# Kernel optimization log

Hardware: AMD Instinct MI355X
Metric: run time of the kernel (lower is better)

## Reference

```python
import jax, jax.numpy as jnp
import numpy as np

NUM_HEADS = 8
LN_EPS = 1e-5


def _avg_pool_mat(n_in, n_out):
    # torch adaptive_avg_pool windows: start=floor(i*n_in/n_out), end=ceil((i+1)*n_in/n_out)
    M = np.zeros((n_out, n_in), dtype=np.float32)
    for i in range(n_out):
        s = (i * n_in) // n_out
        e = -((-(i + 1) * n_in) // n_out)
        M[i, s:e] = 1.0 / (e - s)
    return jnp.asarray(M)


def _adaptive_avg_pool(x, out_hw):
    # separable mean over rectangular windows: [B,C,H,W] -> [B,C,out,out]
    Mh = _avg_pool_mat(x.shape[2], out_hw)
    Mw = _avg_pool_mat(x.shape[3], out_hw)
    return jnp.einsum('bchw,ph,qw->bcpq', x, Mh, Mw)


def _max_pool(x, oh, ow):
    # exact (divisible) adaptive max pool
    B, C, H, W = x.shape
    assert H % oh == 0 and W % ow == 0
    return x.reshape(B, C, oh, H // oh, ow, W // ow).max(axis=(3, 5))


def _conv1x1_res(t, w, b):
    # t + Conv2d(1x1)(t); w is [C_in, C_out]
    return t + jnp.einsum('bchw,cd->bdhw', t, w) + b[None, :, None, None]


def _tokens(t):
    B, C = t.shape[:2]
    return t.reshape(B, C, -1).transpose(0, 2, 1)  # [B, hw, C]


def setup_inputs():
    B, L, C = 8, 1024, 512
    H = W = 64
    key = jax.random.key(0)
    ks = jax.random.split(key, 16)
    n = lambda k, s, sc=0.02: jax.random.normal(k, s, jnp.float32) * sc
    return dict(
        x=jax.random.normal(ks[0], (B, H * W, C), jnp.float32),
        m=jax.random.normal(ks[1], (B, L, C), jnp.float32),
        w_s1=n(ks[2], (C, C)), b_s1=n(ks[3], (C,)),
        w_s2=n(ks[4], (C, C)), b_s2=n(ks[5], (C,)),
        w_s3=n(ks[6], (C, C)), b_s3=n(ks[7], (C,)),
        w_s4=n(ks[8], (C, C)), b_s4=n(ks[9], (C,)),
        w_mx=n(ks[10], (C, C)), b_mx=n(ks[11], (C,)),
        ln_g=jnp.ones((C,), jnp.float32), ln_b=jnp.zeros((C,), jnp.float32),
        Wq=n(ks[12], (C, C)), Wkv=n(ks[13], (C, 2 * C)),
        Wp=n(ks[14], (C, C)), bp=n(ks[15], (C,)),
        H=H, W=W, patch_size=16,
    )


def reference(x, m, w_s1, b_s1, w_s2, b_s2, w_s3, b_s3, w_s4, b_s4,
              w_mx, b_mx, ln_g, ln_b, Wq, Wkv, Wp, bp, H, W, patch_size):
    B, L, C = m.shape
    nh = NUM_HEADS
    d = C // nh
    scale = d ** -0.5

    q = (m @ Wq).reshape(B, L, nh, d).transpose(0, 2, 1, 3)  # [B,nh,L,d]

    x_ = x.transpose(0, 2, 1).reshape(B, C, H, W)
    s1 = _conv1x1_res(_adaptive_avg_pool(x_, round(H * 4 / 12)), w_s1, b_s1)
    s2 = _conv1x1_res(_adaptive_avg_pool(x_, round(H * 4 / 16)), w_s2, b_s2)
    s3 = _conv1x1_res(_adaptive_avg_pool(x_, round(H * 4 / 20)), w_s3, b_s3)
    s4 = _conv1x1_res(_adaptive_avg_pool(x_, round(H * 4 / 24)), w_s4, b_s4)
    mx = _conv1x1_res(_max_pool(x_, H * 4 // patch_size, W * 4 // patch_size), w_mx, b_mx)

    p = jnp.concatenate([_tokens(s1), _tokens(s2), _tokens(s3), _tokens(s4), _tokens(mx)], axis=1)
    mu = p.mean(-1, keepdims=True)
    var = ((p - mu) ** 2).mean(-1, keepdims=True)
    p = (p - mu) / jnp.sqrt(var + LN_EPS) * ln_g + ln_b

    kv_in = jnp.concatenate([p, m], axis=1)  # [B, N_p+L, C]
    kv = (kv_in @ Wkv).reshape(B, -1, 2, nh, d)
    k = kv[:, :, 0].transpose(0, 2, 1, 3)  # [B,nh,N,d]
    v = kv[:, :, 1].transpose(0, 2, 1, 3)

    attn = jax.nn.softmax(jnp.einsum('bhld,bhnd->bhln', q, k) * scale, axis=-1)
    out = jnp.einsum('bhln,bhnd->bhld', attn, v).transpose(0, 2, 1, 3).reshape(B, L, C)
    out = out @ Wp + bp
    return out, mx
```

## Files before the change

### kernel.cpp

```cpp
#include <hip/hip_runtime.h>

typedef unsigned short u16;
typedef __attribute__((ext_vector_type(8))) short bf16x8;
typedef __attribute__((ext_vector_type(4))) float f32x4;

__device__ __forceinline__ float bf2f(u16 u) {
  union { unsigned int i; float f; } x; x.i = ((unsigned int)u) << 16; return x.f;
}
__device__ __forceinline__ u16 f2bf(float f) {
  union { float f; unsigned int i; } x; x.f = f;
  unsigned int r = x.i + 0x7fffu + ((x.i >> 16) & 1u);
  return (u16)(r >> 16);
}

#define CFENCE() asm volatile("" ::: "memory")

__global__ __launch_bounds__(256) void k_pool(
    const float* __restrict__ x, u16* __restrict__ pool)
{
  int blk = blockIdx.x;
  int b = blk / 1243;
  int tok = blk - b * 1243;
  int c = threadIdx.x;
  const float* xb = x + (size_t)b * 4096 * 512;
  float r0, r1;
  if (tok >= 987) {
    int t = tok - 987;
    int oh = t >> 4, ow = t & 15;
    float m0 = -1e38f, m1 = -1e38f;
    for (int hh = 0; hh < 4; hh++)
      for (int ww = 0; ww < 4; ww++) {
        const float* px = xb + (size_t)((oh * 4 + hh) * 64 + ow * 4 + ww) * 512 + c;
        m0 = fmaxf(m0, px[0]);
        m1 = fmaxf(m1, px[256]);
      }
    r0 = m0; r1 = m1;
  } else {
    int n, t;
    if (tok < 441)      { n = 21; t = tok; }
    else if (tok < 697) { n = 16; t = tok - 441; }
    else if (tok < 866) { n = 13; t = tok - 697; }
    else                { n = 11; t = tok - 866; }
    int oh = t / n, ow = t - oh * n;
    int h0 = (oh * 64) / n, h1 = ((oh + 1) * 64 + n - 1) / n;
    int w0 = (ow * 64) / n, w1 = ((ow + 1) * 64 + n - 1) / n;
    float inv = 1.0f / (float)((h1 - h0) * (w1 - w0));
    float s0 = 0.f, s1 = 0.f;
    for (int hh = h0; hh < h1; hh++)
      for (int ww = w0; ww < w1; ww++) {
        const float* px = xb + (size_t)(hh * 64 + ww) * 512 + c;
        s0 += px[0];
        s1 += px[256];
      }
    r0 = s0 * inv; r1 = s1 * inv;
  }
  u16* dst = pool + (size_t)(b * 1243 + tok) * 512 + c;
  dst[0]   = f2bf(r0);
  dst[256] = f2bf(r1);
}

__global__ __launch_bounds__(256) void k_wt8(
    const float* w0, const float* w1, const float* w2, const float* w3,
    const float* w4, const float* w5, const float* w6, const float* w7,
    u16* __restrict__ wt_base)
{
  int z = blockIdx.z;
  int N = (z == 6) ? 1024 : 512;
  if (N == 512 && blockIdx.x >= 16) return;
  const float* W =
      z == 0 ? w0 : z == 1 ? w1 : z == 2 ? w2 : z == 3 ? w3 :
      z == 4 ? w4 : z == 5 ? w5 : z == 6 ? w6 : w7;
  size_t doff = (z <= 5) ? (size_t)z * 262144
                         : (z == 6 ? (size_t)6 * 262144 : (size_t)6 * 262144 + 524288);
  u16* Wt = wt_base + doff;

  __shared__ float tile[32][33];
  int n0 = blockIdx.x * 32, k0 = blockIdx.y * 32;
  int t = threadIdx.x;
  int rr = t >> 5, cc = t & 31;
#pragma unroll
  for (int ps = 0; ps < 4; ps++)
    tile[ps * 8 + rr][cc] = W[(size_t)(k0 + ps * 8 + rr) * N + n0 + cc];
  __syncthreads();
#pragma unroll
  for (int ps = 0; ps < 4; ps++)
    Wt[(size_t)(n0 + ps * 8 + rr) * 512 + k0 + cc] = f2bf(tile[cc][ps * 8 + rr]);
}

__global__ __launch_bounds__(256) void k_f2b(
    const float* __restrict__ src, u16* __restrict__ dst)
{
  size_t i = ((size_t)blockIdx.x * 256 + threadIdx.x) * 8;
  float4 a = *(const float4*)(src + i);
  float4 b = *(const float4*)(src + i + 4);
  ushort4 u0, u1;
  u0.x = f2bf(a.x); u0.y = f2bf(a.y); u0.z = f2bf(a.z); u0.w = f2bf(a.w);
  u1.x = f2bf(b.x); u1.y = f2bf(b.y); u1.z = f2bf(b.z); u1.w = f2bf(b.w);
  *(ushort4*)(dst + i) = u0;
  *(ushort4*)(dst + i + 4) = u1;
}

template <class EPI>
__device__ __forceinline__ void gemm_core(
    const u16* __restrict__ Az, const u16* __restrict__ Bt,
    int M, int K, int m0, int n0, EPI&& epi)
{
  __shared__ __align__(16) u16 As[128][40];
  __shared__ __align__(16) u16 Bs[128][40];

  const int tid = threadIdx.x;
  const int lane = tid & 63, wv = tid >> 6;
  const int quad = lane >> 4, l15 = lane & 15;
  const int wm = (wv >> 1) * 64, wn = (wv & 1) * 64;

  f32x4 acc[4][4];
#pragma unroll
  for (int i = 0; i < 4; i++)
#pragma unroll
    for (int j = 0; j < 4; j++) acc[i][j] = (f32x4){0.f, 0.f, 0.f, 0.f};

  const int srow = tid >> 1;
  const int scol = (tid & 1) * 16;
  const bool aok = (m0 + srow) < M;
  const u16* ag = Az + (size_t)(m0 + srow) * K + scol;
  const u16* bg = Bt + (size_t)(n0 + srow) * K + scol;

  uint4 a0 = {0, 0, 0, 0}, a1 = {0, 0, 0, 0}, b0, b1;
  if (aok) { a0 = *(const uint4*)ag; a1 = *(const uint4*)(ag + 8); }
  b0 = *(const uint4*)bg;
  b1 = *(const uint4*)(bg + 8);

  for (int k0 = 0; k0 < K; k0 += 32) {
    CFENCE();
    __builtin_amdgcn_s_barrier();
    asm volatile("s_waitcnt vmcnt(0)" ::: "memory");
    *(uint4*)&As[srow][scol]     = a0;
    *(uint4*)&As[srow][scol + 8] = a1;
    *(uint4*)&Bs[srow][scol]     = b0;
    *(uint4*)&Bs[srow][scol + 8] = b1;
    if (k0 + 32 < K) {
      if (aok) { a0 = *(const uint4*)(ag + k0 + 32); a1 = *(const uint4*)(ag + k0 + 40); }
      b0 = *(const uint4*)(bg + k0 + 32);
      b1 = *(const uint4*)(bg + k0 + 40);
    }
    asm volatile("s_waitcnt lgkmcnt(0)" ::: "memory");
    __builtin_amdgcn_s_barrier();
    CFENCE();

    bf16x8 af[4];
#pragma unroll
    for (int i = 0; i < 4; i++)
      af[i] = *(const bf16x8*)&As[wm + i * 16 + l15][quad * 8];
#pragma unroll
    for (int j = 0; j < 4; j++) {
      bf16x8 bfj = *(const bf16x8*)&Bs[wn + j * 16 + l15][quad * 8];
#pragma unroll
      for (int i = 0; i < 4; i++)
        acc[i][j] = __builtin_amdgcn_mfma_f32_16x16x32_bf16(af[i], bfj, acc[i][j], 0, 0, 0);
    }
  }

#pragma unroll
  for (int i = 0; i < 4; i++) {
    int rb = m0 + wm + i * 16 + quad * 4;
#pragma unroll
    for (int j = 0; j < 4; j++) {
      int col = n0 + wn + j * 16 + l15;
#pragma unroll
      for (int r = 0; r < 4; r++) {
        int row = rb + r;
        if (row >= M) continue;
        epi(row, col, acc[i][j][r]);
      }
    }
  }
}

__global__ __launch_bounds__(256) void k_gemm_bf(
    const u16* __restrict__ A, long long a_bs, const u16* __restrict__ Bt,
    u16* __restrict__ C, long long c_bs, int M, int N, int K)
{
  const u16* Az = A + (size_t)blockIdx.z * a_bs;
  u16* Cz = C + (size_t)blockIdx.z * c_bs;
  gemm_core(Az, Bt, M, K, blockIdx.y * 128, blockIdx.x * 128,
            [&](int row, int col, float v) {
              Cz[(size_t)row * N + col] = f2bf(v);
            });
}

__global__ __launch_bounds__(256) void k_gemm_f32(
    const u16* __restrict__ A, long long a_bs, const u16* __restrict__ Bt,
    const float* __restrict__ bias, float* __restrict__ C, long long c_bs,
    int M, int N, int K)
{
  const u16* Az = A + (size_t)blockIdx.z * a_bs;
  float* Cz = C + (size_t)blockIdx.z * c_bs;
  gemm_core(Az, Bt, M, K, blockIdx.y * 128, blockIdx.x * 128,
            [&](int row, int col, float v) {
              Cz[(size_t)row * N + col] = v + bias[col];
            });
}

__global__ __launch_bounds__(256) void k_gemm_qkv(
    const u16* __restrict__ mb, const u16* __restrict__ Bt,
    u16* __restrict__ q, u16* __restrict__ KV)
{
  int bz = blockIdx.z;
  const u16* Az = mb + (size_t)bz * (1024 * 512);
  u16* qz  = q  + (size_t)bz * (1024 * 512);
  u16* kvz = KV + (size_t)(bz * 2267 + 1243) * 1024;
  gemm_core(Az, Bt, 1024, 512, blockIdx.y * 128, blockIdx.x * 128,
            [&](int row, int col, float v) {
              u16 bv = f2bf(v);
              if (col < 512) qz[(size_t)row * 512 + col] = bv;
              else           kvz[(size_t)row * 1024 + (col - 512)] = bv;
            });
}

__global__ __launch_bounds__(256) void k_conv_seg(
    const u16* __restrict__ pool, const u16* __restrict__ wts,
    const float* b0, const float* b1, const float* b2, const float* b3,
    const float* b4, u16* __restrict__ p)
{
  int y = blockIdx.y;
  int s, m0;
  if (y < 4)      { s = 0; m0 = y * 128; }
  else if (y < 6) { s = 1; m0 = (y - 4) * 128; }
  else if (y < 8) { s = 2; m0 = (y - 6) * 128; }
  else if (y < 9) { s = 3; m0 = 0; }
  else            { s = 4; m0 = (y - 9) * 128; }
  int t0  = s == 0 ? 0 : s == 1 ? 441 : s == 2 ? 697 : s == 3 ? 866 : 987;
  int cnt = s == 0 ? 441 : s == 1 ? 256 : s == 2 ? 169 : s == 3 ? 121 : 256;
  const float* bias = s == 0 ? b0 : s == 1 ? b1 : s == 2 ? b2 : s == 3 ? b3 : b4;
  size_t base = (size_t)blockIdx.z * (1243 * 512) + (size_t)t0 * 512;
  const u16* Az = pool + base;
  u16* Cz = p + base;
  gemm_core(Az, wts + (size_t)s * 262144, cnt, 512, m0, blockIdx.x * 128,
            [&](int row, int col, float v) {
              v += bias[col] + bf2f(Az[(size_t)row * 512 + col]);
              Cz[(size_t)row * 512 + col] = f2bf(v);
            });
}

__global__ __launch_bounds__(256) void k_ln(
    u16* __restrict__ p, const float* __restrict__ g, const float* __restrict__ bb)
{
  __shared__ float red[8];
  size_t row = blockIdx.x;
  u16* pr = p + row * 512;
  int t = threadIdx.x;
  float v0 = bf2f(pr[t]), v1 = bf2f(pr[t + 256]);
  float s = v0 + v1;
#pragma unroll
  for (int off = 1; off < 64; off <<= 1) s += __shfl_xor(s, off);
  int wave = t >> 6;
  if ((t & 63) == 0) red[wave] = s;
  __syncthreads();
  float mean = (red[0] + red[1] + red[2] + red[3]) * (1.f / 512.f);
  float d0 = v0 - mean, d1 = v1 - mean;
  float s2 = d0 * d0 + d1 * d1;
#pragma unroll
  for (int off = 1; off < 64; off <<= 1) s2 += __shfl_xor(s2, off);
  if ((t & 63) == 0) red[4 + wave] = s2;
  __syncthreads();
  float var = (red[4] + red[5] + red[6] + red[7]) * (1.f / 512.f);
  float rstd = rsqrtf(var + 1e-5f);
  pr[t]       = f2bf(d0 * rstd * g[t]       + bb[t]);
  pr[t + 256] = f2bf(d1 * rstd * g[t + 256] + bb[t + 256]);
}

__global__ __launch_bounds__(256) void k_mxout(
    const u16* __restrict__ p, float* __restrict__ out2)
{
  __shared__ float tile[64][65];
  int tt = blockIdx.x;
  int cc = blockIdx.y;
  int b  = blockIdx.z;
  int tid = threadIdx.x;
  for (int rep = 0; rep < 16; rep++) {
    int e = rep * 256 + tid;
    int r = e >> 6, c = e & 63;
    tile[r][c] = bf2f(p[((size_t)(b * 1243 + 987 + tt * 64 + r)) * 512 + cc * 64 + c]);
  }
  __syncthreads();
  for (int rep = 0; rep < 16; rep++) {
    int e = rep * 256 + tid;
    int crow = e >> 6, tpos = e & 63;
    out2[((size_t)(b * 512 + cc * 64 + crow)) * 256 + tt * 64 + tpos] = tile[tpos][crow];
  }
}

__global__ __launch_bounds__(512) void k_attn_mfma(
    const u16* __restrict__ qb, const u16* __restrict__ KV,
    u16* __restrict__ outb)
{
  __shared__ __align__(16) u16 smem[4][64][72];
#define Qs_ (smem[0])
#define Ks_ (smem[1])
#define Vt_ (smem[2])
#define Ps_ (smem[3])

  const int bid = blockIdx.x;
  const int qt = bid >> 6;
  const int hb = bid & 63;
  const int h = hb & 7, b = hb >> 3;
  const int tid = threadIdx.x;
  const int lane = tid & 63, wv = tid >> 6;
  const int qw = wv >> 1, kw = wv & 1;
  const int quad = lane >> 4, l15 = lane & 15;

  const u16* kvb = KV + (size_t)b * 2267 * 1024;
  const int kr = tid >> 3, kc = (tid & 7) * 8;
  const int vp = tid & 31, vc = (tid >> 5) * 4;

  uint4 kreg = {0, 0, 0, 0};
  uint2 vra = {0, 0}, vrb = {0, 0};
  auto load_tile = [&](int n0) {
    kreg = (uint4){0, 0, 0, 0};
    vra = (uint2){0, 0};
    vrb = (uint2){0, 0};
    if (n0 + kr < 2267)
      kreg = *(const uint4*)(kvb + (size_t)(n0 + kr) * 1024 + h * 64 + kc);
    int na = n0 + 2 * vp;
    const u16* s = kvb + (size_t)na * 1024 + 512 + h * 64 + vc;
    if (na < 2267)     vra = *(const uint2*)s;
    if (na + 1 < 2267) vrb = *(const uint2*)(s + 1024);
  };

  load_tile(0);
  {
    int r = tid >> 3, c = (tid & 7) * 8;
    *(uint4*)&Qs_[r][c] =
        *(const uint4*)(qb + (size_t)(b * 1024 + qt * 64 + r) * 512 + h * 64 + c);
  }

  float l_lane[4];
  f32x4 o_acc[4];
#pragma unroll
  for (int i = 0; i < 4; i++) { l_lane[i] = 0.f; o_acc[i] = (f32x4){0.f, 0.f, 0.f, 0.f}; }

  __syncthreads();

  for (int n0 = 0; n0 < 2267; n0 += 64) {
    CFENCE();
    __builtin_amdgcn_s_barrier();
    asm volatile("s_waitcnt vmcnt(0)" ::: "memory");
    *(uint4*)&Ks_[kr][kc] = kreg;
    {
      unsigned lo0 = __builtin_amdgcn_perm(vrb.x, vra.x, 0x05040100u);
      unsigned hi0 = __builtin_amdgcn_perm(vrb.x, vra.x, 0x07060302u);
      unsigned lo1 = __builtin_amdgcn_perm(vrb.y, vra.y, 0x05040100u);
      unsigned hi1 = __builtin_amdgcn_perm(vrb.y, vra.y, 0x07060302u);
      *(unsigned*)&Vt_[vc + 0][2 * vp] = lo0;
      *(unsigned*)&Vt_[vc + 1][2 * vp] = hi0;
      *(unsigned*)&Vt_[vc + 2][2 * vp] = lo1;
      *(unsigned*)&Vt_[vc + 3][2 * vp] = hi1;
    }
    if (n0 + 64 < 2267) load_tile(n0 + 64);
    asm volatile("s_waitcnt lgkmcnt(0)" ::: "memory");
    __builtin_amdgcn_s_barrier();
    CFENCE();

    bf16x8 aq0 = *(const bf16x8*)&Qs_[qw * 16 + l15][quad * 8];
    bf16x8 aq1 = *(const bf16x8*)&Qs_[qw * 16 + l15][32 + quad * 8];
    f32x4 sacc[2];
#pragma unroll
    for (int t = 0; t < 2; t++) {
      int krow = kw * 32 + t * 16 + l15;
      bf16x8 bk0 = *(const bf16x8*)&Ks_[krow][quad * 8];
      bf16x8 bk1 = *(const bf16x8*)&Ks_[krow][32 + quad * 8];
      f32x4 z = (f32x4){0.f, 0.f, 0.f, 0.f};
      z = __builtin_amdgcn_mfma_f32_16x16x32_bf16(aq0, bk0, z, 0, 0, 0);
      sacc[t] = __builtin_amdgcn_mfma_f32_16x16x32_bf16(aq1, bk1, z, 0, 0, 0);
    }

#pragma unroll
    for (int r = 0; r < 4; r++) {
      float ls = 0.f;
#pragma unroll
      for (int t = 0; t < 2; t++) {
        float e = __builtin_amdgcn_exp2f(fminf(sacc[t][r] * 0.18033688f, 43.28f));
        ls += e;
        Ps_[qw * 16 + quad * 4 + r][kw * 32 + t * 16 + l15] = f2bf(e);
      }
      l_lane[r] += ls;
    }

    bf16x8 ap = *(const bf16x8*)&Ps_[qw * 16 + l15][kw * 32 + quad * 8];
#pragma unroll
    for (int t = 0; t < 4; t++) {
      bf16x8 vf = *(const bf16x8*)&Vt_[t * 16 + l15][kw * 32 + quad * 8];
      o_acc[t] = __builtin_amdgcn_mfma_f32_16x16x32_bf16(ap, vf, o_acc[t], 0, 0, 0);
    }
  }

  float lw[4];
#pragma unroll
  for (int r = 0; r < 4; r++) {
    float l = l_lane[r];
#pragma unroll
    for (int off = 1; off < 16; off <<= 1) l += __shfl_xor(l, off);
    lw[r] = l;
  }

  __syncthreads();
  float* Op = (float*)&smem[0][0][0];
  float* Lp = (float*)&smem[2][0][0];
  if (kw == 1) {
#pragma unroll
    for (int t = 0; t < 4; t++)
#pragma unroll
      for (int r = 0; r < 4; r++)
        Op[(qw * 16 + quad * 4 + r) * 64 + t * 16 + l15] = o_acc[t][r];
    if (l15 == 0) {
#pragma unroll
      for (int r = 0; r < 4; r++) Lp[qw * 16 + quad * 4 + r] = lw[r];
    }
  }
  __syncthreads();
  if (kw == 0) {
#pragma unroll
    for (int r = 0; r < 4; r++) {
      int row = qw * 16 + quad * 4 + r;
      float l = lw[r] + Lp[row] - 37.f;
      float inv = 1.f / fmaxf(l, 1e-20f);
#pragma unroll
      for (int t = 0; t < 4; t++) {
        size_t oi = (size_t)(b * 1024 + qt * 64 + row) * 512 + h * 64 + t * 16 + l15;
        outb[oi] = f2bf((o_acc[t][r] + Op[row * 64 + t * 16 + l15]) * inv);
      }
    }
  }
#undef Qs_
#undef Ks_
#undef Vt_
#undef Ps_
}

extern "C" void kernel_launch(void* const* d_in, const int* in_sizes, int n_in,
                              void* d_out, int out_size, void* d_ws, size_t ws_size,
                              hipStream_t stream)
{
  const float* x = (const float*)d_in[0];
  const float* m = (const float*)d_in[1];
  const float* ln_g = (const float*)d_in[12];
  const float* ln_b = (const float*)d_in[13];
  const float* Wq   = (const float*)d_in[14];
  const float* Wkv  = (const float*)d_in[15];
  const float* Wp   = (const float*)d_in[16];
  const float* bp   = (const float*)d_in[17];
  float* out = (float*)d_out;

  u16* pool = (u16*)d_ws;
  u16* p    = pool + 5091328;
  u16* q    = p + 5091328;
  u16* KV   = q + 4194304;
  u16* mb   = KV + 18571264;
  u16* wt_s = mb + 4194304;
  u16* attn_out = pool;

  k_wt8<<<dim3(32, 16, 8), 256, 0, stream>>>(
      (const float*)d_in[2], (const float*)d_in[4], (const float*)d_in[6],
      (const float*)d_in[8], (const float*)d_in[10], Wq, Wkv, Wp, wt_s);
  k_f2b<<<2048, 256, 0, stream>>>(m, mb);

  k_pool<<<9944, 256, 0, stream>>>(x, pool);

  k_conv_seg<<<dim3(4, 11, 8), 256, 0, stream>>>(
      pool, wt_s, (const float*)d_in[3], (const float*)d_in[5],
      (const float*)d_in[7], (const float*)d_in[9], (const float*)d_in[11], p);

  k_mxout<<<dim3(4, 8, 8), 256, 0, stream>>>(p, out + 4194304);
  k_ln<<<9944, 256, 0, stream>>>(p, ln_g, ln_b);

  k_gemm_qkv<<<dim3(12, 8, 8), 256, 0, stream>>>(mb, wt_s + 5 * 262144, q, KV);

  k_gemm_bf<<<dim3(8, 10, 8), 256, 0, stream>>>(p, (long long)1243 * 512,
                                                wt_s + 6 * 262144,
                                                KV, (long long)2267 * 1024,
                                                1243, 1024, 512);

  k_attn_mfma<<<1024, 512, 0, stream>>>(q, KV, attn_out);

  k_gemm_f32<<<dim3(4, 8, 8), 256, 0, stream>>>(attn_out, (long long)1024 * 512,
                                                wt_s + 6 * 262144 + 524288, bp,
                                                out, (long long)1024 * 512,
                                                1024, 512, 512);
  (void)in_sizes; (void)n_in; (void)out_size; (void)ws_size;
}
```

Before: 412.4 us.

## Fuse small launches and streamline attention softmax with DPP transposes

Folds the m-to-bf16 conversion into the pooling launch, writes the transposed max-pool output straight from the conv epilogue, and merges the QKV and pooled-KV GEMMs into one launch, removing three kernel launches and a separate transpose pass. In attention, Q fragments are loaded directly into registers instead of through shared memory, and the probability tile is packed with DPP quad transposes plus v_cvt_pk_bf16 into wider LDS stores, with a cheaper row-sum reduction. The out2 writes from the conv epilogue are strided (uncoalesced), and the merged GEMM grid wastes some blocks that exit early.

```diff
diff --git a/kernel.cpp b/kernel.cpp
--- a/kernel.cpp
+++ b/kernel.cpp
@@ -15,10 +15,36 @@
 
 #define CFENCE() asm volatile("" ::: "memory")
 
+__device__ __forceinline__ float qpB1(float v) {
+  return __builtin_bit_cast(float, __builtin_amdgcn_update_dpp(
+      0, __builtin_bit_cast(int, v), 0xB1, 0xF, 0xF, true));
+}
+__device__ __forceinline__ float qp4E(float v) {
+  return __builtin_bit_cast(float, __builtin_amdgcn_update_dpp(
+      0, __builtin_bit_cast(int, v), 0x4E, 0xF, 0xF, true));
+}
+__device__ __forceinline__ unsigned cvtpk_bf16(float lo, float hi) {
+  unsigned r;
+  asm("v_cvt_pk_bf16_f32 %0, %1, %2" : "=v"(r) : "v"(lo), "v"(hi));
+  return r;
+}
+
 __global__ __launch_bounds__(256) void k_pool(
-    const float* __restrict__ x, u16* __restrict__ pool)
+    const float* __restrict__ x, u16* __restrict__ pool,
+    const float* __restrict__ m, u16* __restrict__ mb)
 {
   int blk = blockIdx.x;
+  if (blk >= 9944) {
+    size_t i = ((size_t)(blk - 9944) * 256 + threadIdx.x) * 8;
+    float4 a = *(const float4*)(m + i);
+    float4 b = *(const float4*)(m + i + 4);
+    ushort4 u0, u1;
+    u0.x = f2bf(a.x); u0.y = f2bf(a.y); u0.z = f2bf(a.z); u0.w = f2bf(a.w);
+    u1.x = f2bf(b.x); u1.y = f2bf(b.y); u1.z = f2bf(b.z); u1.w = f2bf(b.w);
+    *(ushort4*)(mb + i) = u0;
+    *(ushort4*)(mb + i + 4) = u1;
+    return;
+  }
   int b = blk / 1243;
   int tok = blk - b * 1243;
   int c = threadIdx.x;
@@ -87,19 +113,6 @@
     Wt[(size_t)(n0 + ps * 8 + rr) * 512 + k0 + cc] = f2bf(tile[cc][ps * 8 + rr]);
 }
 
-__global__ __launch_bounds__(256) void k_f2b(
-    const float* __restrict__ src, u16* __restrict__ dst)
-{
-  size_t i = ((size_t)blockIdx.x * 256 + threadIdx.x) * 8;
-  float4 a = *(const float4*)(src + i);
-  float4 b = *(const float4*)(src + i + 4);
-  ushort4 u0, u1;
-  u0.x = f2bf(a.x); u0.y = f2bf(a.y); u0.z = f2bf(a.z); u0.w = f2bf(a.w);
-  u1.x = f2bf(b.x); u1.y = f2bf(b.y); u1.z = f2bf(b.z); u1.w = f2bf(b.w);
-  *(ushort4*)(dst + i) = u0;
-  *(ushort4*)(dst + i + 4) = u1;
-}
-
 template <class EPI>
 __device__ __forceinline__ void gemm_core(
     const u16* __restrict__ Az, const u16* __restrict__ Bt,
@@ -176,18 +189,6 @@
   }
 }
 
-__global__ __launch_bounds__(256) void k_gemm_bf(
-    const u16* __restrict__ A, long long a_bs, const u16* __restrict__ Bt,
-    u16* __restrict__ C, long long c_bs, int M, int N, int K)
-{
-  const u16* Az = A + (size_t)blockIdx.z * a_bs;
-  u16* Cz = C + (size_t)blockIdx.z * c_bs;
-  gemm_core(Az, Bt, M, K, blockIdx.y * 128, blockIdx.x * 128,
-            [&](int row, int col, float v) {
-              Cz[(size_t)row * N + col] = f2bf(v);
-            });
-}
-
 __global__ __launch_bounds__(256) void k_gemm_f32(
     const u16* __restrict__ A, long long a_bs, const u16* __restrict__ Bt,
     const float* __restrict__ bias, float* __restrict__ C, long long c_bs,
@@ -201,28 +202,39 @@
             });
 }
 
-__global__ __launch_bounds__(256) void k_gemm_qkv(
-    const u16* __restrict__ mb, const u16* __restrict__ Bt,
+__global__ __launch_bounds__(256) void k_gemm_big(
+    const u16* __restrict__ mb, const u16* __restrict__ p,
+    const u16* __restrict__ wqkv, const u16* __restrict__ wkv,
     u16* __restrict__ q, u16* __restrict__ KV)
 {
-  int bz = blockIdx.z;
-  const u16* Az = mb + (size_t)bz * (1024 * 512);
-  u16* qz  = q  + (size_t)bz * (1024 * 512);
-  u16* kvz = KV + (size_t)(bz * 2267 + 1243) * 1024;
-  gemm_core(Az, Bt, 1024, 512, blockIdx.y * 128, blockIdx.x * 128,
-            [&](int row, int col, float v) {
-              u16 bv = f2bf(v);
-              if (col < 512) qz[(size_t)row * 512 + col] = bv;
-              else           kvz[(size_t)row * 1024 + (col - 512)] = bv;
-            });
+  int y = blockIdx.y, z = blockIdx.z;
+  if (y < 8) {
+    const u16* Az = mb + (size_t)z * (1024 * 512);
+    u16* qz  = q  + (size_t)z * (1024 * 512);
+    u16* kvz = KV + (size_t)(z * 2267 + 1243) * 1024;
+    gemm_core(Az, wqkv, 1024, 512, y * 128, blockIdx.x * 128,
+              [&](int row, int col, float v) {
+                u16 bv = f2bf(v);
+                if (col < 512) qz[(size_t)row * 512 + col] = bv;
+                else           kvz[(size_t)row * 1024 + (col - 512)] = bv;
+              });
+  } else {
+    if (blockIdx.x >= 8) return;
+    const u16* Az = p + (size_t)z * (1243 * 512);
+    u16* kvz = KV + (size_t)z * 2267 * 1024;
+    gemm_core(Az, wkv, 1243, 512, (y - 8) * 128, blockIdx.x * 128,
+              [&](int row, int col, float v) {
+                kvz[(size_t)row * 1024 + col] = f2bf(v);
+              });
+  }
 }
 
 __global__ __launch_bounds__(256) void k_conv_seg(
     const u16* __restrict__ pool, const u16* __restrict__ wts,
     const float* b0, const float* b1, const float* b2, const float* b3,
-    const float* b4, u16* __restrict__ p)
-{
-  int y = blockIdx.y;
+    const float* b4, u16* __restrict__ p, float* __restrict__ out2)
+{
+  int y = blockIdx.y, bz = blockIdx.z;
   int s, m0;
   if (y < 4)      { s = 0; m0 = y * 128; }
   else if (y < 6) { s = 1; m0 = (y - 4) * 128; }
@@ -232,13 +244,15 @@
   int t0  = s == 0 ? 0 : s == 1 ? 441 : s == 2 ? 697 : s == 3 ? 866 : 987;
   int cnt = s == 0 ? 441 : s == 1 ? 256 : s == 2 ? 169 : s == 3 ? 121 : 256;
   const float* bias = s == 0 ? b0 : s == 1 ? b1 : s == 2 ? b2 : s == 3 ? b3 : b4;
-  size_t base = (size_t)blockIdx.z * (1243 * 512) + (size_t)t0 * 512;
+  size_t base = (size_t)bz * (1243 * 512) + (size_t)t0 * 512;
   const u16* Az = pool + base;
   u16* Cz = p + base;
   gemm_core(Az, wts + (size_t)s * 262144, cnt, 512, m0, blockIdx.x * 128,
             [&](int row, int col, float v) {
               v += bias[col] + bf2f(Az[(size_t)row * 512 + col]);
               Cz[(size_t)row * 512 + col] = f2bf(v);
+              if (s == 4)
+                out2[((size_t)(bz * 512 + col)) * 256 + row] = v;
             });
 }
 
@@ -269,36 +283,14 @@
   pr[t + 256] = f2bf(d1 * rstd * g[t + 256] + bb[t + 256]);
 }
 
-__global__ __launch_bounds__(256) void k_mxout(
-    const u16* __restrict__ p, float* __restrict__ out2)
-{
-  __shared__ float tile[64][65];
-  int tt = blockIdx.x;
-  int cc = blockIdx.y;
-  int b  = blockIdx.z;
-  int tid = threadIdx.x;
-  for (int rep = 0; rep < 16; rep++) {
-    int e = rep * 256 + tid;
-    int r = e >> 6, c = e & 63;
-    tile[r][c] = bf2f(p[((size_t)(b * 1243 + 987 + tt * 64 + r)) * 512 + cc * 64 + c]);
-  }
-  __syncthreads();
-  for (int rep = 0; rep < 16; rep++) {
-    int e = rep * 256 + tid;
-    int crow = e >> 6, tpos = e & 63;
-    out2[((size_t)(b * 512 + cc * 64 + crow)) * 256 + tt * 64 + tpos] = tile[tpos][crow];
-  }
-}
-
 __global__ __launch_bounds__(512) void k_attn_mfma(
     const u16* __restrict__ qb, const u16* __restrict__ KV,
     u16* __restrict__ outb)
 {
-  __shared__ __align__(16) u16 smem[4][64][72];
-#define Qs_ (smem[0])
-#define Ks_ (smem[1])
-#define Vt_ (smem[2])
-#define Ps_ (smem[3])
+  __shared__ __align__(16) u16 KsV[2][64][72];
+  __shared__ __align__(16) u16 Psm[64][72];
+#define Ks_ (KsV[0])
+#define Vt_ (KsV[1])
 
   const int bid = blockIdx.x;
   const int qt = bid >> 6;
@@ -328,18 +320,16 @@
   };
 
   load_tile(0);
-  {
-    int r = tid >> 3, c = (tid & 7) * 8;
-    *(uint4*)&Qs_[r][c] =
-        *(const uint4*)(qb + (size_t)(b * 1024 + qt * 64 + r) * 512 + h * 64 + c);
-  }
-
-  float l_lane[4];
+  const u16* qrow = qb + (size_t)(b * 1024 + qt * 64 + qw * 16 + l15) * 512 + h * 64;
+  bf16x8 aq0 = *(const bf16x8*)(qrow + quad * 8);
+  bf16x8 aq1 = *(const bf16x8*)(qrow + 32 + quad * 8);
+
+  float l_acc = 0.f;
   f32x4 o_acc[4];
 #pragma unroll
-  for (int i = 0; i < 4; i++) { l_lane[i] = 0.f; o_acc[i] = (f32x4){0.f, 0.f, 0.f, 0.f}; }
-
-  __syncthreads();
+  for (int i = 0; i < 4; i++) o_acc[i] = (f32x4){0.f, 0.f, 0.f, 0.f};
+
+  const bool o1 = (lane & 1) != 0, o2 = (lane & 2) != 0;
 
   for (int n0 = 0; n0 < 2267; n0 += 64) {
     CFENCE();
@@ -361,8 +351,6 @@
     __builtin_amdgcn_s_barrier();
     CFENCE();
 
-    bf16x8 aq0 = *(const bf16x8*)&Qs_[qw * 16 + l15][quad * 8];
-    bf16x8 aq1 = *(const bf16x8*)&Qs_[qw * 16 + l15][32 + quad * 8];
     f32x4 sacc[2];
 #pragma unroll
     for (int t = 0; t < 2; t++) {
@@ -375,18 +363,24 @@
     }
 
 #pragma unroll
-    for (int r = 0; r < 4; r++) {
-      float ls = 0.f;
-#pragma unroll
-      for (int t = 0; t < 2; t++) {
-        float e = __builtin_amdgcn_exp2f(fminf(sacc[t][r] * 0.18033688f, 43.28f));
-        ls += e;
-        Ps_[qw * 16 + quad * 4 + r][kw * 32 + t * 16 + l15] = f2bf(e);
-      }
-      l_lane[r] += ls;
-    }
-
-    bf16x8 ap = *(const bf16x8*)&Ps_[qw * 16 + l15][kw * 32 + quad * 8];
+    for (int t = 0; t < 2; t++) {
+      float v0 = __builtin_amdgcn_exp2f(fminf(sacc[t][0] * 0.18033688f, 43.28f));
+      float v1 = __builtin_amdgcn_exp2f(fminf(sacc[t][1] * 0.18033688f, 43.28f));
+      float v2 = __builtin_amdgcn_exp2f(fminf(sacc[t][2] * 0.18033688f, 43.28f));
+      float v3 = __builtin_amdgcn_exp2f(fminf(sacc[t][3] * 0.18033688f, 43.28f));
+      float x, y;
+      x = o1 ? v0 : v1; y = qpB1(x); v0 = o1 ? y : v0; v1 = o1 ? v1 : y;
+      x = o1 ? v2 : v3; y = qpB1(x); v2 = o1 ? y : v2; v3 = o1 ? v3 : y;
+      x = o2 ? v0 : v2; y = qp4E(x); v0 = o2 ? y : v0; v2 = o2 ? v2 : y;
+      x = o2 ? v1 : v3; y = qp4E(x); v1 = o2 ? y : v1; v3 = o2 ? v3 : y;
+      l_acc += (v0 + v1) + (v2 + v3);
+      uint2 d;
+      d.x = cvtpk_bf16(v0, v1);
+      d.y = cvtpk_bf16(v2, v3);
+      *(uint2*)&Psm[qw * 16 + quad * 4 + (l15 & 3)][kw * 32 + t * 16 + (l15 & 12)] = d;
+    }
+
+    bf16x8 ap = *(const bf16x8*)&Psm[qw * 16 + l15][kw * 32 + quad * 8];
 #pragma unroll
     for (int t = 0; t < 4; t++) {
       bf16x8 vf = *(const bf16x8*)&Vt_[t * 16 + l15][kw * 32 + quad * 8];
@@ -394,36 +388,29 @@
     }
   }
 
-  float lw[4];
-#pragma unroll
-  for (int r = 0; r < 4; r++) {
-    float l = l_lane[r];
-#pragma unroll
-    for (int off = 1; off < 16; off <<= 1) l += __shfl_xor(l, off);
-    lw[r] = l;
-  }
+  float l = l_acc;
+  l += __shfl_xor(l, 4);
+  l += __shfl_xor(l, 8);
 
   __syncthreads();
-  float* Op = (float*)&smem[0][0][0];
-  float* Lp = (float*)&smem[2][0][0];
+  float* Op = (float*)&KsV[0][0][0];
+  float* Lp = (float*)&Psm[0][0];
   if (kw == 1) {
 #pragma unroll
     for (int t = 0; t < 4; t++)
 #pragma unroll
       for (int r = 0; r < 4; r++)
         Op[(qw * 16 + quad * 4 + r) * 64 + t * 16 + l15] = o_acc[t][r];
-    if (l15 == 0) {
-#pragma unroll
-      for (int r = 0; r < 4; r++) Lp[qw * 16 + quad * 4 + r] = lw[r];
-    }
+    if (l15 < 4) Lp[qw * 16 + quad * 4 + l15] = l;
   }
   __syncthreads();
   if (kw == 0) {
 #pragma unroll
     for (int r = 0; r < 4; r++) {
+      float lr = __shfl(l, (lane & 60) | r);
       int row = qw * 16 + quad * 4 + r;
-      float l = lw[r] + Lp[row] - 37.f;
-      float inv = 1.f / fmaxf(l, 1e-20f);
+      float lt = lr + Lp[row] - 37.f;
+      float inv = 1.f / fmaxf(lt, 1e-20f);
 #pragma unroll
       for (int t = 0; t < 4; t++) {
         size_t oi = (size_t)(b * 1024 + qt * 64 + row) * 512 + h * 64 + t * 16 + l15;
@@ -431,10 +418,8 @@
       }
     }
   }
-#undef Qs_
 #undef Ks_
 #undef Vt_
-#undef Ps_
 }
 
 extern "C" void kernel_launch(void* const* d_in, const int* in_sizes, int n_in,
@@ -462,23 +447,18 @@
   k_wt8<<<dim3(32, 16, 8), 256, 0, stream>>>(
       (const float*)d_in[2], (const float*)d_in[4], (const float*)d_in[6],
       (const float*)d_in[8], (const float*)d_in[10], Wq, Wkv, Wp, wt_s);
-  k_f2b<<<2048, 256, 0, stream>>>(m, mb);
-
-  k_pool<<<9944, 256, 0, stream>>>(x, pool);
+
+  k_pool<<<11992, 256, 0, stream>>>(x, pool, m, mb);
 
   k_conv_seg<<<dim3(4, 11, 8), 256, 0, stream>>>(
       pool, wt_s, (const float*)d_in[3], (const float*)d_in[5],
-      (const float*)d_in[7], (const float*)d_in[9], (const float*)d_in[11], p);
-
-  k_mxout<<<dim3(4, 8, 8), 256, 0, stream>>>(p, out + 4194304);
+      (const float*)d_in[7], (const float*)d_in[9], (const float*)d_in[11],
+      p, out + 4194304);
+
   k_ln<<<9944, 256, 0, stream>>>(p, ln_g, ln_b);
 
-  k_gemm_qkv<<<dim3(12, 8, 8), 256, 0, stream>>>(mb, wt_s + 5 * 262144, q, KV);
-
-  k_gemm_bf<<<dim3(8, 10, 8), 256, 0, stream>>>(p, (long long)1243 * 512,
-                                                wt_s + 6 * 262144,
-                                                KV, (long long)2267 * 1024,
-                                                1243, 1024, 512);
+  k_gemm_big<<<dim3(12, 18, 8), 256, 0, stream>>>(
+      mb, p, wt_s + 5 * 262144, wt_s + 6 * 262144, q, KV);
 
   k_attn_mfma<<<1024, 512, 0, stream>>>(q, KV, attn_out);
 
```

Result: no change. 409.3 us (-0.7%).
